# Optimization experiments

Hardware: AMD Instinct MI355X
Metric: run time of the kernel (lower is better)

The kernel has to match this reference:

```python
import jax, jax.numpy as jnp
import numpy as np

CODEBOOK_SIZE = 8192
DIM = 256
COMMITMENT_COST = 0.25


def setup_inputs() -> dict:
    key = jax.random.key(0)
    k1, k2 = jax.random.split(key)
    z = jax.random.normal(k1, (8, DIM, 1024), dtype=jnp.float32)
    # nn.init.uniform_(codebook.weight, -1/K, 1/K)
    bound = 1.0 / CODEBOOK_SIZE
    codebook = jax.random.uniform(k2, (CODEBOOK_SIZE, DIM), dtype=jnp.float32,
                                  minval=-bound, maxval=bound)
    return {"z": z, "codebook": codebook}


def reference(z, codebook):
    B, D, T = z.shape
    z_perm = jnp.transpose(z, (0, 2, 1)).reshape(B * T, D)  # (BT, D)
    # ||z||^2 - 2 z.c + ||c||^2  -> (BT, K)
    distances = (jnp.sum(z_perm * z_perm, axis=1, keepdims=True)
                 - 2.0 * (z_perm @ codebook.T)
                 + jnp.sum(codebook * codebook, axis=1)[None, :])
    indices = jnp.argmin(distances, axis=1)          # (BT,)
    z_q_flat = codebook[indices]                     # (BT, D)
    z_q = jnp.transpose(z_q_flat.reshape(B, T, D), (0, 2, 1))  # (B, D, T)

    codebook_loss = jnp.mean((z_q - jax.lax.stop_gradient(z)) ** 2)
    commitment_loss = COMMITMENT_COST * jnp.mean((jax.lax.stop_gradient(z_q) - z) ** 2)
    loss = codebook_loss + commitment_loss

    # straight-through estimator
    z_q_st = z + jax.lax.stop_gradient(z_q - z)
    return z_q_st, indices.reshape(B, T), loss
```

## Files before the change

### kernel.cpp

```cpp
#include <hip/hip_runtime.h>

#define DD   256
#define TT   1024
#define BT   8192
#define KK   8192
#define ZQ_SIZE 2097152

#define FLT_INF 3.402823466e38f

typedef __attribute__((ext_vector_type(8))) short short8;
typedef __attribute__((ext_vector_type(4))) float f32x4;

#define ASP_B   0u
#define BSP_B   12582912u
#define AN_B    25165824u
#define CN_B    25198592u
#define KEY_B   25231360u
#define ACC_B   25296896u

static __device__ __forceinline__ unsigned short f2bf(float x) {
    unsigned int u = __float_as_uint(x);
    return (unsigned short)((u + 0x7FFF + ((u >> 16) & 1)) >> 16);
}
static __device__ __forceinline__ float bf2f(unsigned short h) {
    return __uint_as_float(((unsigned int)h) << 16);
}
static __device__ __forceinline__ void split3(float x, unsigned short& h,
                                              unsigned short& m, unsigned short& l) {
    h = f2bf(x);
    float r1 = x - bf2f(h);
    m = f2bf(r1);
    l = f2bf(r1 - bf2f(m));
}

static __device__ __forceinline__ void gld16(const void* g, const void* l) {
    __builtin_amdgcn_global_load_lds(
        (const __attribute__((address_space(1))) unsigned int*)g,
        (__attribute__((address_space(3))) unsigned int*)l, 16, 0, 0);
}

__global__ __launch_bounds__(256) void vq_prep(const float* __restrict__ z,
                                               const float* __restrict__ cb,
                                               float* __restrict__ An,
                                               unsigned short* __restrict__ Asp,
                                               unsigned short* __restrict__ Bsp,
                                               float* __restrict__ Cn,
                                               unsigned long long* __restrict__ keys,
                                               float* __restrict__ lacc) {
    __shared__ float T[64][257];
    int tid = threadIdx.x;
    if (blockIdx.x < 32) {
        int g = blockIdx.x * 256 + tid;
        int b = g >> 10, t = g & 1023;
        const float* zp = z + (size_t)b * (DD * TT) + t;
        float s = 0.f;
        #pragma unroll 8
        for (int d = 0; d < DD; ++d) {
            float v = zp[d * TT];
            float v2 = v * v;
            s = s + v2;
        }
        An[g] = s;
        keys[g] = ~0ull;
        if (g == 0) *lacc = 0.f;
    } else if (blockIdx.x < 32 + 2048) {
        int g = (blockIdx.x - 32) * 256 + tid;
        int code = g >> 6, d4 = (g & 63) * 4;
        float4 v = *(const float4*)&cb[(size_t)code * DD + d4];
        unsigned short h[4], m[4], l[4];
        split3(v.x, h[0], m[0], l[0]);
        split3(v.y, h[1], m[1], l[1]);
        split3(v.z, h[2], m[2], l[2]);
        split3(v.w, h[3], m[3], l[3]);
        unsigned short* row = Bsp + (size_t)code * 768 + d4;
        *(ushort4*)&row[0]   = make_ushort4(h[0], h[1], h[2], h[3]);
        *(ushort4*)&row[256] = make_ushort4(m[0], m[1], m[2], m[3]);
        *(ushort4*)&row[512] = make_ushort4(l[0], l[1], l[2], l[3]);
        float s = v.x * v.x + v.y * v.y + v.z * v.z + v.w * v.w;
        #pragma unroll
        for (int off = 32; off; off >>= 1) s += __shfl_down(s, off, 64);
        if ((tid & 63) == 0) Cn[code] = s;
    } else {
        int blk = blockIdx.x - 2080;
        int b = blk >> 4;
        int t0 = (blk & 15) * 64;
        #pragma unroll
        for (int it = 0; it < 16; ++it) {
            int d = it * 16 + (tid >> 4);
            int t4 = (tid & 15) * 4;
            float4 v = *(const float4*)&z[(size_t)b * (DD * TT) + (size_t)d * TT + t0 + t4];
            T[t4 + 0][d] = v.x; T[t4 + 1][d] = v.y; T[t4 + 2][d] = v.z; T[t4 + 3][d] = v.w;
        }
        __syncthreads();
        int r = tid >> 2, q = tid & 3;
        int token = b * 1024 + t0 + r;
        unsigned short* arow = Asp + (size_t)token * 768;
        #pragma unroll
        for (int dd = 0; dd < 16; ++dd) {
            int d = dd * 16 + q * 4;
            unsigned short h[4], m[4], l[4];
            #pragma unroll
            for (int c = 0; c < 4; ++c) split3(T[r][d + c], h[c], m[c], l[c]);
            *(ushort4*)&arow[d]       = make_ushort4(h[0], h[1], h[2], h[3]);
            *(ushort4*)&arow[256 + d] = make_ushort4(m[0], m[1], m[2], m[3]);
            *(ushort4*)&arow[512 + d] = make_ushort4(l[0], l[1], l[2], l[3]);
        }
    }
}

__global__ __launch_bounds__(1024, 4) void vq_scores(const unsigned short* __restrict__ Asp,
                                                     const unsigned short* __restrict__ Bsp,
                                                     const float* __restrict__ An,
                                                     const float* __restrict__ Cn,
                                                     unsigned long long* __restrict__ keys) {
    __shared__ __attribute__((aligned(16))) unsigned short lds[2][32768];

    int bid = blockIdx.x;
    int g = bid >> 6, sl = bid & 63;
    int mt = (g >> 2) * 8 + (sl >> 3);
    int nt = (g & 3) * 8 + (sl & 7);
    const int token0 = mt * 256, code0 = nt * 256;

    const int wid = threadIdx.x >> 6, lane = threadIdx.x & 63;
    const int m0w = (wid >> 2) * 64, n0w = (wid & 3) * 64;

    const int srl = lane >> 3;
    const int gslot = (lane & 7) ^ (srl & 7);
    const size_t arow = (size_t)(token0 + wid * 16 + srl) * 768 + gslot * 8;
    const size_t brow = (size_t)(code0 + wid * 16 + srl) * 768 + gslot * 8;
    const int ldsrow = (wid * 16) * 64;

    f32x4 acc[4][4];
    #pragma unroll
    for (int i = 0; i < 4; ++i)
        #pragma unroll
        for (int j = 0; j < 4; ++j) acc[i][j] = (f32x4){0.f, 0.f, 0.f, 0.f};

    {
        #pragma unroll
        for (int n = 0; n < 2; ++n) {
            gld16(Asp + arow + (size_t)(n * 8) * 768, &lds[0][ldsrow + n * 8 * 64]);
            gld16(Bsp + brow + (size_t)(n * 8) * 768, &lds[0][16384 + ldsrow + n * 8 * 64]);
        }
    }

    for (int t = 0; t < 24; ++t) {
        __syncthreads();
        if (t < 23) {
            int c = (t + 1) >> 2, kk = (t + 1) & 3;
            int ka = ((0x120100 >> (c * 4)) & 15) * 256 + kk * 64;
            int kb = ((0x102010 >> (c * 4)) & 15) * 256 + kk * 64;
            int p = (t + 1) & 1;
            #pragma unroll
            for (int n = 0; n < 2; ++n) {
                gld16(Asp + arow + (size_t)(n * 8) * 768 + ka,
                      &lds[p][ldsrow + n * 8 * 64]);
                gld16(Bsp + brow + (size_t)(n * 8) * 768 + kb,
                      &lds[p][16384 + ldsrow + n * 8 * 64]);
            }
        }
        const unsigned short* A = &lds[t & 1][0];
        const unsigned short* B = &lds[t & 1][16384];

        #pragma unroll
        for (int h = 0; h < 2; ++h) {
            short8 af[4], bf[4];
            const int s0 = h * 4 + (lane >> 4);
            #pragma unroll
            for (int i = 0; i < 4; ++i) {
                int row = m0w + i * 16 + (lane & 15);
                af[i] = *(const short8*)&A[row * 64 + ((s0 ^ (row & 7)) * 8)];
            }
            #pragma unroll
            for (int j = 0; j < 4; ++j) {
                int row = n0w + j * 16 + (lane & 15);
                bf[j] = *(const short8*)&B[row * 64 + ((s0 ^ (row & 7)) * 8)];
            }
            #pragma unroll
            for (int i = 0; i < 4; ++i)
                #pragma unroll
                for (int j = 0; j < 4; ++j)
                    acc[i][j] = __builtin_amdgcn_mfma_f32_16x16x32_bf16(
                        af[i], bf[j], acc[i][j], 0, 0, 0);
        }
    }

    const int quad = lane >> 4, col = lane & 15;
    float cn[4]; int cidx[4];
    #pragma unroll
    for (int j = 0; j < 4; ++j) {
        cidx[j] = code0 + n0w + j * 16 + col;
        cn[j] = Cn[cidx[j]];
    }
    #pragma unroll
    for (int i = 0; i < 4; ++i) {
        #pragma unroll
        for (int r = 0; r < 4; ++r) {
            int token = token0 + m0w + i * 16 + quad * 4 + r;
            float Ai = An[token];
            float bv = FLT_INF; int bi = 0;
            #pragma unroll
            for (int j = 0; j < 4; ++j) {
                float d1 = fmaf(-2.f, acc[i][j][r], Ai);
                float dist = d1 + cn[j];
                if (dist < bv) { bv = dist; bi = cidx[j]; }
            }
            #pragma unroll
            for (int off = 8; off; off >>= 1) {
                float ov = __shfl_down(bv, off, 16);
                int   oi = __shfl_down(bi, off, 16);
                if (ov < bv || (ov == bv && oi < bi)) { bv = ov; bi = oi; }
            }
            if (col == 0) {
                unsigned long long key =
                    ((unsigned long long)__float_as_uint(bv) << 32) | (unsigned)bi;
                atomicMin(&keys[token], key);
            }
        }
    }
}

__global__ __launch_bounds__(256) void vq_gather(const float* __restrict__ z,
                                                 const float* __restrict__ cb,
                                                 const unsigned long long* __restrict__ keys,
                                                 float* __restrict__ out,
                                                 float* __restrict__ out_idx,
                                                 float* __restrict__ loss_acc) {
    int e4 = blockIdx.x * 256 + threadIdx.x;
    int t4 = e4 & 255;
    int rest = e4 >> 8;
    int d = rest & 255;
    int b = rest >> 8;
    int gbase = b * 1024 + t4 * 4;

    const int* klo = (const int*)keys;
    int i0 = klo[(size_t)(gbase + 0) * 2];
    int i1 = klo[(size_t)(gbase + 1) * 2];
    int i2 = klo[(size_t)(gbase + 2) * 2];
    int i3 = klo[(size_t)(gbase + 3) * 2];
    if (d == 0) {
        out_idx[gbase + 0] = (float)i0;
        out_idx[gbase + 1] = (float)i1;
        out_idx[gbase + 2] = (float)i2;
        out_idx[gbase + 3] = (float)i3;
    }

    float4 zv = *(const float4*)&z[(size_t)e4 * 4];
    float q0 = cb[(size_t)i0 * DD + d];
    float q1 = cb[(size_t)i1 * DD + d];
    float q2 = cb[(size_t)i2 * DD + d];
    float q3 = cb[(size_t)i3 * DD + d];

    float d0 = q0 - zv.x, d1 = q1 - zv.y, d2 = q2 - zv.z, d3 = q3 - zv.w;
    float4 o;
    o.x = zv.x + d0; o.y = zv.y + d1; o.z = zv.z + d2; o.w = zv.w + d3;
    *(float4*)&out[(size_t)e4 * 4] = o;

    float s = d0 * d0 + d1 * d1 + d2 * d2 + d3 * d3;
    #pragma unroll
    for (int off = 32; off; off >>= 1) s += __shfl_down(s, off, 64);
    __shared__ float wsum[4];
    if ((threadIdx.x & 63) == 0) wsum[threadIdx.x >> 6] = s;
    __syncthreads();
    if (threadIdx.x == 0)
        atomicAdd(loss_acc, wsum[0] + wsum[1] + wsum[2] + wsum[3]);
}

__global__ void vq_loss(const float* __restrict__ loss_acc, float* __restrict__ out_loss) {
    *out_loss = 1.25f * (*loss_acc) / 2097152.f;
}

extern "C" void kernel_launch(void* const* d_in, const int* in_sizes, int n_in,
                              void* d_out, int out_size, void* d_ws, size_t ws_size,
                              hipStream_t stream) {
    const float* z  = (const float*)d_in[0];
    const float* cb = (const float*)d_in[1];
    float* out = (float*)d_out;
    char*  w   = (char*)d_ws;

    unsigned short* Asp = (unsigned short*)(w + ASP_B);
    unsigned short* Bsp = (unsigned short*)(w + BSP_B);
    float* An = (float*)(w + AN_B);
    float* Cn = (float*)(w + CN_B);
    unsigned long long* keys = (unsigned long long*)(w + KEY_B);
    float* lacc = (float*)(w + ACC_B);

    vq_prep   <<<32 + 2048 + 128, 256, 0, stream>>>(z, cb, An, Asp, Bsp, Cn, keys, lacc);
    vq_scores <<<1024, 1024, 0, stream>>>(Asp, Bsp, An, Cn, keys);
    vq_gather <<<ZQ_SIZE / 1024, 256, 0, stream>>>(z, cb, keys, out, out + ZQ_SIZE, lacc);
    vq_loss   <<<1, 1, 0, stream>>>(lacc, out + ZQ_SIZE + BT);
}
```

Before: 321.0 us.

## Use 8 waves with 64x128 warp tiles in scores GEMM; fold loss kernel into gather

```diff
diff --git a/kernel.cpp b/kernel.cpp
--- a/kernel.cpp
+++ b/kernel.cpp
@@ -17,6 +17,7 @@
 #define CN_B    25198592u
 #define KEY_B   25231360u
 #define ACC_B   25296896u
+#define CNT_B   25296900u
 
 static __device__ __forceinline__ unsigned short f2bf(float x) {
     unsigned int u = __float_as_uint(x);
@@ -46,15 +47,17 @@
                                                unsigned short* __restrict__ Bsp,
                                                float* __restrict__ Cn,
                                                unsigned long long* __restrict__ keys,
-                                               float* __restrict__ lacc) {
+                                               float* __restrict__ lacc,
+                                               unsigned int* __restrict__ counter) {
     __shared__ float T[64][257];
     int tid = threadIdx.x;
-    if (blockIdx.x < 32) {
-        int g = blockIdx.x * 256 + tid;
+    if (blockIdx.x < 128) {
+        if (tid >= 64) return;
+        int g = blockIdx.x * 64 + tid;
         int b = g >> 10, t = g & 1023;
         const float* zp = z + (size_t)b * (DD * TT) + t;
         float s = 0.f;
-        #pragma unroll 8
+        #pragma unroll 16
         for (int d = 0; d < DD; ++d) {
             float v = zp[d * TT];
             float v2 = v * v;
@@ -62,9 +65,9 @@
         }
         An[g] = s;
         keys[g] = ~0ull;
-        if (g == 0) *lacc = 0.f;
-    } else if (blockIdx.x < 32 + 2048) {
-        int g = (blockIdx.x - 32) * 256 + tid;
+        if (g == 0) { *lacc = 0.f; *counter = 0u; }
+    } else if (blockIdx.x < 128 + 2048) {
+        int g = (blockIdx.x - 128) * 256 + tid;
         int code = g >> 6, d4 = (g & 63) * 4;
         float4 v = *(const float4*)&cb[(size_t)code * DD + d4];
         unsigned short h[4], m[4], l[4];
@@ -81,7 +84,7 @@
         for (int off = 32; off; off >>= 1) s += __shfl_down(s, off, 64);
         if ((tid & 63) == 0) Cn[code] = s;
     } else {
-        int blk = blockIdx.x - 2080;
+        int blk = blockIdx.x - 2176;
         int b = blk >> 4;
         int t0 = (blk & 15) * 64;
         #pragma unroll
@@ -108,11 +111,11 @@
     }
 }
 
-__global__ __launch_bounds__(1024, 4) void vq_scores(const unsigned short* __restrict__ Asp,
-                                                     const unsigned short* __restrict__ Bsp,
-                                                     const float* __restrict__ An,
-                                                     const float* __restrict__ Cn,
-                                                     unsigned long long* __restrict__ keys) {
+__global__ __launch_bounds__(512, 2) void vq_scores(const unsigned short* __restrict__ Asp,
+                                                    const unsigned short* __restrict__ Bsp,
+                                                    const float* __restrict__ An,
+                                                    const float* __restrict__ Cn,
+                                                    unsigned long long* __restrict__ keys) {
     __shared__ __attribute__((aligned(16))) unsigned short lds[2][32768];
 
     int bid = blockIdx.x;
@@ -122,26 +125,25 @@
     const int token0 = mt * 256, code0 = nt * 256;
 
     const int wid = threadIdx.x >> 6, lane = threadIdx.x & 63;
-    const int m0w = (wid >> 2) * 64, n0w = (wid & 3) * 64;
+    const int m0w = (wid >> 1) * 64;
+    const int n0w = (wid & 1) * 128;
 
     const int srl = lane >> 3;
-    const int gslot = (lane & 7) ^ (srl & 7);
-    const size_t arow = (size_t)(token0 + wid * 16 + srl) * 768 + gslot * 8;
-    const size_t brow = (size_t)(code0 + wid * 16 + srl) * 768 + gslot * 8;
-    const int ldsrow = (wid * 16) * 64;
-
-    f32x4 acc[4][4];
+    const int gslot = (lane & 7) ^ srl;
+    const size_t arow = (size_t)(token0 + wid * 32 + srl) * 768 + gslot * 8;
+    const size_t brow = (size_t)(code0 + wid * 32 + srl) * 768 + gslot * 8;
+    const int ldsrow = (wid * 32) * 64;
+
+    f32x4 acc[4][8];
     #pragma unroll
     for (int i = 0; i < 4; ++i)
         #pragma unroll
-        for (int j = 0; j < 4; ++j) acc[i][j] = (f32x4){0.f, 0.f, 0.f, 0.f};
-
-    {
-        #pragma unroll
-        for (int n = 0; n < 2; ++n) {
-            gld16(Asp + arow + (size_t)(n * 8) * 768, &lds[0][ldsrow + n * 8 * 64]);
-            gld16(Bsp + brow + (size_t)(n * 8) * 768, &lds[0][16384 + ldsrow + n * 8 * 64]);
-        }
+        for (int j = 0; j < 8; ++j) acc[i][j] = (f32x4){0.f, 0.f, 0.f, 0.f};
+
+    #pragma unroll
+    for (int n = 0; n < 4; ++n) {
+        gld16(Asp + arow + (size_t)(n * 8) * 768, &lds[0][ldsrow + n * 8 * 64]);
+        gld16(Bsp + brow + (size_t)(n * 8) * 768, &lds[0][16384 + ldsrow + n * 8 * 64]);
     }
 
     for (int t = 0; t < 24; ++t) {
@@ -152,7 +154,7 @@
             int kb = ((0x102010 >> (c * 4)) & 15) * 256 + kk * 64;
             int p = (t + 1) & 1;
             #pragma unroll
-            for (int n = 0; n < 2; ++n) {
+            for (int n = 0; n < 4; ++n) {
                 gld16(Asp + arow + (size_t)(n * 8) * 768 + ka,
                       &lds[p][ldsrow + n * 8 * 64]);
                 gld16(Bsp + brow + (size_t)(n * 8) * 768 + kb,
@@ -164,7 +166,7 @@
 
         #pragma unroll
         for (int h = 0; h < 2; ++h) {
-            short8 af[4], bf[4];
+            short8 af[4], bf[8];
             const int s0 = h * 4 + (lane >> 4);
             #pragma unroll
             for (int i = 0; i < 4; ++i) {
@@ -172,23 +174,23 @@
                 af[i] = *(const short8*)&A[row * 64 + ((s0 ^ (row & 7)) * 8)];
             }
             #pragma unroll
-            for (int j = 0; j < 4; ++j) {
+            for (int j = 0; j < 8; ++j) {
                 int row = n0w + j * 16 + (lane & 15);
                 bf[j] = *(const short8*)&B[row * 64 + ((s0 ^ (row & 7)) * 8)];
             }
             #pragma unroll
             for (int i = 0; i < 4; ++i)
                 #pragma unroll
-                for (int j = 0; j < 4; ++j)
+                for (int j = 0; j < 8; ++j)
                     acc[i][j] = __builtin_amdgcn_mfma_f32_16x16x32_bf16(
                         af[i], bf[j], acc[i][j], 0, 0, 0);
         }
     }
 
     const int quad = lane >> 4, col = lane & 15;
-    float cn[4]; int cidx[4];
-    #pragma unroll
-    for (int j = 0; j < 4; ++j) {
+    float cn[8]; int cidx[8];
+    #pragma unroll
+    for (int j = 0; j < 8; ++j) {
         cidx[j] = code0 + n0w + j * 16 + col;
         cn[j] = Cn[cidx[j]];
     }
@@ -200,7 +202,7 @@
             float Ai = An[token];
             float bv = FLT_INF; int bi = 0;
             #pragma unroll
-            for (int j = 0; j < 4; ++j) {
+            for (int j = 0; j < 8; ++j) {
                 float d1 = fmaf(-2.f, acc[i][j][r], Ai);
                 float dist = d1 + cn[j];
                 if (dist < bv) { bv = dist; bi = cidx[j]; }
@@ -225,7 +227,9 @@
                                                  const unsigned long long* __restrict__ keys,
                                                  float* __restrict__ out,
                                                  float* __restrict__ out_idx,
-                                                 float* __restrict__ loss_acc) {
+                                                 float* __restrict__ loss_acc,
+                                                 unsigned int* __restrict__ counter,
+                                                 float* __restrict__ out_loss) {
     int e4 = blockIdx.x * 256 + threadIdx.x;
     int t4 = e4 & 255;
     int rest = e4 >> 8;
@@ -262,12 +266,15 @@
     __shared__ float wsum[4];
     if ((threadIdx.x & 63) == 0) wsum[threadIdx.x >> 6] = s;
     __syncthreads();
-    if (threadIdx.x == 0)
+    if (threadIdx.x == 0) {
         atomicAdd(loss_acc, wsum[0] + wsum[1] + wsum[2] + wsum[3]);
-}
-
-__global__ void vq_loss(const float* __restrict__ loss_acc, float* __restrict__ out_loss) {
-    *out_loss = 1.25f * (*loss_acc) / 2097152.f;
+        __threadfence();
+        unsigned int n = atomicAdd(counter, 1u);
+        if (n == 2047u) {
+            float total = atomicAdd(loss_acc, 0.f);
+            *out_loss = 1.25f * total / 2097152.f;
+        }
+    }
 }
 
 extern "C" void kernel_launch(void* const* d_in, const int* in_sizes, int n_in,
@@ -284,9 +291,11 @@
     float* Cn = (float*)(w + CN_B);
     unsigned long long* keys = (unsigned long long*)(w + KEY_B);
     float* lacc = (float*)(w + ACC_B);
-
-    vq_prep   <<<32 + 2048 + 128, 256, 0, stream>>>(z, cb, An, Asp, Bsp, Cn, keys, lacc);
-    vq_scores <<<1024, 1024, 0, stream>>>(Asp, Bsp, An, Cn, keys);
-    vq_gather <<<ZQ_SIZE / 1024, 256, 0, stream>>>(z, cb, keys, out, out + ZQ_SIZE, lacc);
-    vq_loss   <<<1, 1, 0, stream>>>(lacc, out + ZQ_SIZE + BT);
-}
+    unsigned int* counter = (unsigned int*)(w + CNT_B);
+
+    vq_prep   <<<128 + 2048 + 128, 256, 0, stream>>>(z, cb, An, Asp, Bsp, Cn, keys,
+                                                     lacc, counter);
+    vq_scores <<<1024, 512, 0, stream>>>(Asp, Bsp, An, Cn, keys);
+    vq_gather <<<ZQ_SIZE / 1024, 256, 0, stream>>>(z, cb, keys, out, out + ZQ_SIZE,
+                                                   lacc, counter, out + ZQ_SIZE + BT);
+}
```

Result: slower. 358.5 us (+11.7%).

## Retile score GEMM to 128x256 blocks with 4 waves and 64x128 warp tiles

Applied to the files above, without the earlier changes.

```diff
diff --git a/kernel.cpp b/kernel.cpp
--- a/kernel.cpp
+++ b/kernel.cpp
@@ -108,87 +108,86 @@
     }
 }
 
-__global__ __launch_bounds__(1024, 4) void vq_scores(const unsigned short* __restrict__ Asp,
-                                                     const unsigned short* __restrict__ Bsp,
-                                                     const float* __restrict__ An,
-                                                     const float* __restrict__ Cn,
-                                                     unsigned long long* __restrict__ keys) {
-    __shared__ __attribute__((aligned(16))) unsigned short lds[2][32768];
+__global__ __launch_bounds__(256, 2) void vq_scores(const unsigned short* __restrict__ Asp,
+                                                    const unsigned short* __restrict__ Bsp,
+                                                    const float* __restrict__ An,
+                                                    const float* __restrict__ Cn,
+                                                    unsigned long long* __restrict__ keys) {
+    __shared__ __attribute__((aligned(16))) unsigned short lds[2][12288];
 
     int bid = blockIdx.x;
     int g = bid >> 6, sl = bid & 63;
     int mt = (g >> 2) * 8 + (sl >> 3);
     int nt = (g & 3) * 8 + (sl & 7);
-    const int token0 = mt * 256, code0 = nt * 256;
+    const int token0 = mt * 128, code0 = nt * 256;
 
     const int wid = threadIdx.x >> 6, lane = threadIdx.x & 63;
-    const int m0w = (wid >> 2) * 64, n0w = (wid & 3) * 64;
-
-    const int srl = lane >> 3;
-    const int gslot = (lane & 7) ^ (srl & 7);
-    const size_t arow = (size_t)(token0 + wid * 16 + srl) * 768 + gslot * 8;
-    const size_t brow = (size_t)(code0 + wid * 16 + srl) * 768 + gslot * 8;
-    const int ldsrow = (wid * 16) * 64;
-
-    f32x4 acc[4][4];
+    const int m0w = (wid >> 1) * 64;
+    const int n0w = (wid & 1) * 128;
+
+    const int srl = lane >> 2;
+    const int gslot = (lane & 3) ^ (srl & 3);
+    const size_t arow = (size_t)(token0 + wid * 32 + srl) * 768 + gslot * 8;
+    const size_t brow = (size_t)(code0 + wid * 64 + srl) * 768 + gslot * 8;
+    const int albase = (wid * 32) * 32;
+    const int blbase = 4096 + (wid * 64) * 32;
+
+    f32x4 acc[4][8];
     #pragma unroll
     for (int i = 0; i < 4; ++i)
         #pragma unroll
-        for (int j = 0; j < 4; ++j) acc[i][j] = (f32x4){0.f, 0.f, 0.f, 0.f};
-
-    {
-        #pragma unroll
-        for (int n = 0; n < 2; ++n) {
-            gld16(Asp + arow + (size_t)(n * 8) * 768, &lds[0][ldsrow + n * 8 * 64]);
-            gld16(Bsp + brow + (size_t)(n * 8) * 768, &lds[0][16384 + ldsrow + n * 8 * 64]);
-        }
-    }
-
-    for (int t = 0; t < 24; ++t) {
+        for (int j = 0; j < 8; ++j) acc[i][j] = (f32x4){0.f, 0.f, 0.f, 0.f};
+
+    #pragma unroll
+    for (int n = 0; n < 2; ++n)
+        gld16(Asp + arow + (size_t)(n * 16) * 768, &lds[0][albase + n * 16 * 32]);
+    #pragma unroll
+    for (int n = 0; n < 4; ++n)
+        gld16(Bsp + brow + (size_t)(n * 16) * 768, &lds[0][blbase + n * 16 * 32]);
+
+    const int quad = lane >> 4, col = lane & 15;
+
+    for (int t = 0; t < 48; ++t) {
         __syncthreads();
-        if (t < 23) {
-            int c = (t + 1) >> 2, kk = (t + 1) & 3;
-            int ka = ((0x120100 >> (c * 4)) & 15) * 256 + kk * 64;
-            int kb = ((0x102010 >> (c * 4)) & 15) * 256 + kk * 64;
+        if (t < 47) {
+            int c = (t + 1) >> 3, kk = (t + 1) & 7;
+            int ka = ((0x120100 >> (c * 4)) & 15) * 256 + kk * 32;
+            int kb = ((0x102010 >> (c * 4)) & 15) * 256 + kk * 32;
             int p = (t + 1) & 1;
             #pragma unroll
-            for (int n = 0; n < 2; ++n) {
-                gld16(Asp + arow + (size_t)(n * 8) * 768 + ka,
-                      &lds[p][ldsrow + n * 8 * 64]);
-                gld16(Bsp + brow + (size_t)(n * 8) * 768 + kb,
-                      &lds[p][16384 + ldsrow + n * 8 * 64]);
-            }
+            for (int n = 0; n < 2; ++n)
+                gld16(Asp + arow + (size_t)(n * 16) * 768 + ka,
+                      &lds[p][albase + n * 16 * 32]);
+            #pragma unroll
+            for (int n = 0; n < 4; ++n)
+                gld16(Bsp + brow + (size_t)(n * 16) * 768 + kb,
+                      &lds[p][blbase + n * 16 * 32]);
         }
         const unsigned short* A = &lds[t & 1][0];
-        const unsigned short* B = &lds[t & 1][16384];
-
-        #pragma unroll
-        for (int h = 0; h < 2; ++h) {
-            short8 af[4], bf[4];
-            const int s0 = h * 4 + (lane >> 4);
-            #pragma unroll
-            for (int i = 0; i < 4; ++i) {
-                int row = m0w + i * 16 + (lane & 15);
-                af[i] = *(const short8*)&A[row * 64 + ((s0 ^ (row & 7)) * 8)];
-            }
-            #pragma unroll
-            for (int j = 0; j < 4; ++j) {
-                int row = n0w + j * 16 + (lane & 15);
-                bf[j] = *(const short8*)&B[row * 64 + ((s0 ^ (row & 7)) * 8)];
-            }
-            #pragma unroll
-            for (int i = 0; i < 4; ++i)
-                #pragma unroll
-                for (int j = 0; j < 4; ++j)
-                    acc[i][j] = __builtin_amdgcn_mfma_f32_16x16x32_bf16(
-                        af[i], bf[j], acc[i][j], 0, 0, 0);
-        }
-    }
-
-    const int quad = lane >> 4, col = lane & 15;
-    float cn[4]; int cidx[4];
-    #pragma unroll
-    for (int j = 0; j < 4; ++j) {
+        const unsigned short* B = &lds[t & 1][4096];
+
+        short8 af[4], bf[8];
+        #pragma unroll
+        for (int i = 0; i < 4; ++i) {
+            int row = m0w + i * 16 + col;
+            af[i] = *(const short8*)&A[row * 32 + ((quad ^ (row & 3)) * 8)];
+        }
+        #pragma unroll
+        for (int j = 0; j < 8; ++j) {
+            int row = n0w + j * 16 + col;
+            bf[j] = *(const short8*)&B[row * 32 + ((quad ^ (row & 3)) * 8)];
+        }
+        #pragma unroll
+        for (int i = 0; i < 4; ++i)
+            #pragma unroll
+            for (int j = 0; j < 8; ++j)
+                acc[i][j] = __builtin_amdgcn_mfma_f32_16x16x32_bf16(
+                    af[i], bf[j], acc[i][j], 0, 0, 0);
+    }
+
+    float cn[8]; int cidx[8];
+    #pragma unroll
+    for (int j = 0; j < 8; ++j) {
         cidx[j] = code0 + n0w + j * 16 + col;
         cn[j] = Cn[cidx[j]];
     }
@@ -200,7 +199,7 @@
             float Ai = An[token];
             float bv = FLT_INF; int bi = 0;
             #pragma unroll
-            for (int j = 0; j < 4; ++j) {
+            for (int j = 0; j < 8; ++j) {
                 float d1 = fmaf(-2.f, acc[i][j][r], Ai);
                 float dist = d1 + cn[j];
                 if (dist < bv) { bv = dist; bi = cidx[j]; }
@@ -286,7 +285,7 @@
     float* lacc = (float*)(w + ACC_B);
 
     vq_prep   <<<32 + 2048 + 128, 256, 0, stream>>>(z, cb, An, Asp, Bsp, Cn, keys, lacc);
-    vq_scores <<<1024, 1024, 0, stream>>>(Asp, Bsp, An, Cn, keys);
+    vq_scores <<<2048, 256, 0, stream>>>(Asp, Bsp, An, Cn, keys);
     vq_gather <<<ZQ_SIZE / 1024, 256, 0, stream>>>(z, cb, keys, out, out + ZQ_SIZE, lacc);
     vq_loss   <<<1, 1, 0, stream>>>(lacc, out + ZQ_SIZE + BT);
 }
```

After: 344.9 us. +7.4%, slower.
